# Kernel optimization log

Hardware: AMD Instinct MI355X
Metric: run time of the kernel (lower is better)

The kernel has to match this reference:

```python
import jax, jax.numpy as jnp
import numpy as np

EPS = 1e-12

def _pairwise_dist(a, b):
    # a: [B,N,3], b: [B,M,3] -> Euclidean distances [B,N,M]
    d2 = (jnp.sum(a * a, -1)[:, :, None]
          + jnp.sum(b * b, -1)[:, None, :]
          - 2.0 * jnp.einsum('bnd,bmd->bnm', a, b))
    return jnp.sqrt(jnp.maximum(d2, EPS))


def setup_inputs() -> dict:
    key = jax.random.key(0)
    k1, k2, k3 = jax.random.split(key, 3)
    B, N, M = 16, 4096, 1024
    shape_xyz = jax.random.normal(k1, (B, N, 6), dtype=jnp.float32)
    skel_xyz = jax.random.normal(k2, (B, M, 3), dtype=jnp.float32)
    skel_nori = jax.random.normal(k3, (B, M, 3), dtype=jnp.float32)
    return {"shape_xyz": shape_xyz, "skel_xyz": skel_xyz, "skel_nori": skel_nori}


def reference(shape_xyz, skel_xyz, skel_nori):
    normal = shape_xyz[:, :, 3:6]          # [B,N,3]
    pts = shape_xyz[:, :, :3]              # [B,N,3]
    B = skel_nori.shape[0]

    # Chamfer-style closest distances (sum of min Euclidean distances, both ways)
    d_shape2skel = _pairwise_dist(pts, skel_xyz)   # [B,N,M]
    cd1 = jnp.sum(jnp.min(d_shape2skel, axis=2))
    cd2 = jnp.sum(jnp.min(d_shape2skel, axis=1))   # same matrix transposed
    loss_cd = (cd1 + cd2) * 0.0001

    # KNN (k=2) of each skeletal point among shape points (cKDTree equivalent)
    d_skel2shape = jnp.transpose(d_shape2skel, (0, 2, 1))  # [B,M,N]
    _, idx = jax.lax.top_k(-d_skel2shape, 2)               # [B,M,2]

    # Gather normals of the 2 nearest shape points: [B,M,2,3]
    knn_normals = jnp.take_along_axis(normal[:, None, :, :],
                                      idx[:, :, :, None], axis=2)
    dots = jnp.einsum('bmd,bmkd->bmk', skel_nori, knn_normals)  # [B,M,2]
    # |dot| averaged over k, summed over (b, j), divided by batch size
    loss_normal = jnp.sum(jnp.mean(jnp.abs(dots), axis=-1)) / B

    return loss_cd + 0.001 * loss_normal
```

## Files before the change

### kernel.cpp

```cpp
#include <hip/hip_runtime.h>
#include <cfloat>
#include <stdint.h>

#define B_ 16
#define N_ 4096
#define M_ 1024
#define EPS_ 1e-12f

__device__ __forceinline__ uint32_t umin3(uint32_t a, uint32_t b, uint32_t c) {
    return min(a, min(b, c));
}
__device__ __forceinline__ uint32_t umed3(uint32_t a, uint32_t b, uint32_t c) {
    return max(min(a, b), min(max(a, b), c));
}

__global__ __launch_bounds__(256, 8) void fused_kernel(const float* __restrict__ shape_xyz,
                                                       const float* __restrict__ skel_xyz,
                                                       const float* __restrict__ skel_nori,
                                                       float* __restrict__ out)
{
    __shared__ float4 ls4[1024];
    __shared__ float ws[4];

    const int role = blockIdx.x & 1;
    const int id   = blockIdx.x >> 1;
    const int b    = id >> 6;
    const int sub  = id & 63;

    float v = 0.0f;

    if (role == 0) {
        const float* skb = skel_xyz + (size_t)b * M_ * 3;
        for (int i = threadIdx.x; i < M_; i += 256) {
            const float x = skb[i * 3 + 0];
            const float y = skb[i * 3 + 1];
            const float z = skb[i * 3 + 2];
            ls4[i] = make_float4(x, y, z, fmaf(x, x, fmaf(y, y, z * z)));
        }
        __syncthreads();

        const int s  = threadIdx.x & 15;
        const int g  = threadIdx.x >> 4;
        const int n0 = sub * 64 + g * 4;

        const float* p = shape_xyz + ((size_t)b * N_ + n0) * 6;
        float m2x[4], m2y[4], m2z[4], pp[4], best[4];
#pragma unroll
        for (int k = 0; k < 4; ++k) {
            const float x = p[k * 6 + 0];
            const float y = p[k * 6 + 1];
            const float z = p[k * 6 + 2];
            m2x[k] = -2.0f * x; m2y[k] = -2.0f * y; m2z[k] = -2.0f * z;
            pp[k]  = fmaf(x, x, fmaf(y, y, z * z));
            best[k] = FLT_MAX;
        }

#pragma unroll 4
        for (int t = 0; t < 32; ++t) {
            const float4 sv0 = ls4[t * 32 + s];
            const float4 sv1 = ls4[t * 32 + 16 + s];
#pragma unroll
            for (int k = 0; k < 4; ++k) {
                const float t0 = fmaf(m2x[k], sv0.x, fmaf(m2y[k], sv0.y, fmaf(m2z[k], sv0.z, sv0.w)));
                const float t1 = fmaf(m2x[k], sv1.x, fmaf(m2y[k], sv1.y, fmaf(m2z[k], sv1.z, sv1.w)));
                best[k] = fminf(best[k], fminf(t0, t1));
            }
        }

#pragma unroll
        for (int off = 1; off < 16; off <<= 1) {
#pragma unroll
            for (int k = 0; k < 4; ++k) best[k] = fminf(best[k], __shfl_xor(best[k], off));
        }
        if (s == 0) {
#pragma unroll
            for (int k = 0; k < 4; ++k) v += sqrtf(fmaxf(best[k] + pp[k], EPS_));
            v *= 1e-4f;
        }
    } else {
        const int s  = threadIdx.x & 63;
        const int w  = threadIdx.x >> 6;
        const int m0 = sub * 16 + w * 4;

        float m2x[4], m2y[4], m2z[4], aa[4];
        uint32_t k1[4], k2[4];
        {
            const float* sq = skel_xyz + ((size_t)b * M_ + m0) * 3;
#pragma unroll
            for (int c = 0; c < 4; ++c) {
                const float x = sq[c * 3 + 0];
                const float y = sq[c * 3 + 1];
                const float z = sq[c * 3 + 2];
                m2x[c] = -2.0f * x; m2y[c] = -2.0f * y; m2z[c] = -2.0f * z;
                aa[c]  = fmaf(x, x, fmaf(y, y, z * z));
                k1[c] = 0xFFFFFFFFu; k2[c] = 0xFFFFFFFFu;
            }
        }

        const uint32_t HI = 0xFFFFF000u;
        const float* sb = shape_xyz + (size_t)b * N_ * 6;

        for (int ph = 0; ph < 4; ++ph) {
            __syncthreads();
            for (int i = threadIdx.x; i < 1024; i += 256) {
                const float* pt = sb + (size_t)(ph * 1024 + i) * 6;
                const float x = pt[0], y = pt[1], z = pt[2];
                ls4[i] = make_float4(x, y, z, fmaf(x, x, fmaf(y, y, z * z)));
            }
            __syncthreads();
            const uint32_t nb = (uint32_t)(ph * 1024);

#pragma unroll 2
            for (int j = 0; j < 8; ++j) {
                const int nl = j * 128 + s;
                const float4 qA = ls4[nl];
                const float4 qB = ls4[nl + 64];
                const uint32_t gnA = nb + (uint32_t)nl;
                const uint32_t gnB = gnA + 64u;
#pragma unroll
                for (int c = 0; c < 4; ++c) {
                    const float tA = fmaf(m2x[c], qA.x, fmaf(m2y[c], qA.y, fmaf(m2z[c], qA.z, qA.w + aa[c])));
                    const float tB = fmaf(m2x[c], qB.x, fmaf(m2y[c], qB.y, fmaf(m2z[c], qB.z, qB.w + aa[c])));
                    const uint32_t kA = (__float_as_uint(tA) & HI) | gnA;
                    const uint32_t kB = (__float_as_uint(tB) & HI) | gnB;
                    k2[c] = min(k2[c], umed3(k1[c], kA, kB));
                    k1[c] = umin3(k1[c], kA, kB);
                }
            }
        }

#pragma unroll
        for (int off = 1; off < 64; off <<= 1) {
#pragma unroll
            for (int c = 0; c < 4; ++c) {
                const uint32_t o1 = (uint32_t)__shfl_xor((int)k1[c], off);
                const uint32_t o2 = (uint32_t)__shfl_xor((int)k2[c], off);
                const uint32_t nk2 = min(min(k2[c], o2), max(k1[c], o1));
                k1[c] = min(k1[c], o1);
                k2[c] = nk2;
            }
        }

        if (s == 0) {
            const float* no = skel_nori + ((size_t)b * M_ + m0) * 3;
            const float kN = 0.001f * 0.5f / (float)B_;
#pragma unroll
            for (int c = 0; c < 4; ++c) {
                const int i1 = (int)(k1[c] & 0xFFFu);
                const int i2 = (int)(k2[c] & 0xFFFu);
                const float* p1 = sb + (size_t)i1 * 6;
                const float* p2 = sb + (size_t)i2 * 6;
                const float ax = -0.5f * m2x[c], ay = -0.5f * m2y[c], az = -0.5f * m2z[c];
                const float dx = ax - p1[0], dy = ay - p1[1], dz = az - p1[2];
                const float d2 = fmaf(dx, dx, fmaf(dy, dy, dz * dz));
                const float q0 = no[c * 3 + 0], q1 = no[c * 3 + 1], q2 = no[c * 3 + 2];
                const float dot1 = q0 * p1[3] + q1 * p1[4] + q2 * p1[5];
                const float dot2 = q0 * p2[3] + q1 * p2[4] + q2 * p2[5];
                v += sqrtf(fmaxf(d2, EPS_)) * 1e-4f + (fabsf(dot1) + fabsf(dot2)) * kN;
            }
        }
    }

#pragma unroll
    for (int off = 32; off > 0; off >>= 1) v += __shfl_down(v, off);
    if ((threadIdx.x & 63) == 0) ws[threadIdx.x >> 6] = v;
    __syncthreads();
    if (threadIdx.x == 0) atomicAdd(out, ws[0] + ws[1] + ws[2] + ws[3]);
}

extern "C" void kernel_launch(void* const* d_in, const int* in_sizes, int n_in,
                              void* d_out, int out_size, void* d_ws, size_t ws_size,
                              hipStream_t stream) {
    const float* shape_xyz = (const float*)d_in[0];
    const float* skel_xyz  = (const float*)d_in[1];
    const float* skel_nori = (const float*)d_in[2];
    float* out = (float*)d_out;

    hipMemsetAsync(out, 0, sizeof(float), stream);
    fused_kernel<<<2048, 256, 0, stream>>>(shape_xyz, skel_xyz, skel_nori, out);
}
```

Measured before the change: 93.26 us.

## Merge both distance passes into every block instead of role-split blocks

Instead of alternating blocks between the shape-to-skeleton min pass and the skeleton-to-shape top-2 pass, every block now does a slice of both: 32 shape points against all skeleton points, then 8 skeleton points against all shape points. Each thread now handles 1 shape point and 2 skeleton queries instead of 4, which lowers register pressure and balances work across blocks. The cost is less register-level reuse of each shared-memory load (fewer FMAs per LDS read) and more staging passes overall, since every block now fills shared memory five times.

Result: slower. 98.18 us (+5.3%).

```diff
diff --git a/kernel.cpp b/kernel.cpp
--- a/kernel.cpp
+++ b/kernel.cpp
@@ -22,142 +22,121 @@
     __shared__ float4 ls4[1024];
     __shared__ float ws[4];
 
-    const int role = blockIdx.x & 1;
-    const int id   = blockIdx.x >> 1;
-    const int b    = id >> 6;
-    const int sub  = id & 63;
+    const int b = blockIdx.x >> 7;
+    const int t = blockIdx.x & 127;
 
     float v = 0.0f;
 
-    if (role == 0) {
-        const float* skb = skel_xyz + (size_t)b * M_ * 3;
-        for (int i = threadIdx.x; i < M_; i += 256) {
-            const float x = skb[i * 3 + 0];
-            const float y = skb[i * 3 + 1];
-            const float z = skb[i * 3 + 2];
+    const float* skb = skel_xyz + (size_t)b * M_ * 3;
+    for (int i = threadIdx.x; i < 1024; i += 256) {
+        const float x = skb[i * 3 + 0];
+        const float y = skb[i * 3 + 1];
+        const float z = skb[i * 3 + 2];
+        ls4[i] = make_float4(x, y, z, fmaf(x, x, fmaf(y, y, z * z)));
+    }
+    __syncthreads();
+
+    {
+        const int sA = threadIdx.x & 7;
+        const int gA = threadIdx.x >> 3;
+        const float* p = shape_xyz + ((size_t)b * N_ + t * 32 + gA) * 6;
+        const float px = p[0], py = p[1], pz = p[2];
+        const float m2x = -2.0f * px, m2y = -2.0f * py, m2z = -2.0f * pz;
+        const float pp  = fmaf(px, px, fmaf(py, py, pz * pz));
+
+        float best = FLT_MAX;
+#pragma unroll 4
+        for (int j = 0; j < 64; ++j) {
+            const float4 s0 = ls4[j * 16 + sA];
+            const float4 s1 = ls4[j * 16 + 8 + sA];
+            const float t0 = fmaf(m2x, s0.x, fmaf(m2y, s0.y, fmaf(m2z, s0.z, s0.w)));
+            const float t1 = fmaf(m2x, s1.x, fmaf(m2y, s1.y, fmaf(m2z, s1.z, s1.w)));
+            best = fminf(best, fminf(t0, t1));
+        }
+#pragma unroll
+        for (int off = 1; off < 8; off <<= 1) best = fminf(best, __shfl_xor(best, off));
+        if (sA == 0) v += sqrtf(fmaxf(best + pp, EPS_)) * 1e-4f;
+    }
+
+    const int sB = threadIdx.x & 63;
+    const int w  = threadIdx.x >> 6;
+    const int m0 = t * 8 + w * 2;
+
+    float m2x[2], m2y[2], m2z[2], aa[2];
+    uint32_t k1[2], k2[2];
+    {
+        const float* sq = skel_xyz + ((size_t)b * M_ + m0) * 3;
+#pragma unroll
+        for (int c = 0; c < 2; ++c) {
+            const float x = sq[c * 3 + 0];
+            const float y = sq[c * 3 + 1];
+            const float z = sq[c * 3 + 2];
+            m2x[c] = -2.0f * x; m2y[c] = -2.0f * y; m2z[c] = -2.0f * z;
+            aa[c]  = fmaf(x, x, fmaf(y, y, z * z));
+            k1[c] = 0xFFFFFFFFu; k2[c] = 0xFFFFFFFFu;
+        }
+    }
+
+    const uint32_t HI = 0xFFFFF000u;
+    const float* sb = shape_xyz + (size_t)b * N_ * 6;
+
+    for (int ph = 0; ph < 4; ++ph) {
+        __syncthreads();
+        for (int i = threadIdx.x; i < 1024; i += 256) {
+            const float* pt = sb + (size_t)(ph * 1024 + i) * 6;
+            const float x = pt[0], y = pt[1], z = pt[2];
             ls4[i] = make_float4(x, y, z, fmaf(x, x, fmaf(y, y, z * z)));
         }
         __syncthreads();
+        const uint32_t nb = (uint32_t)(ph * 1024);
 
-        const int s  = threadIdx.x & 15;
-        const int g  = threadIdx.x >> 4;
-        const int n0 = sub * 64 + g * 4;
-
-        const float* p = shape_xyz + ((size_t)b * N_ + n0) * 6;
-        float m2x[4], m2y[4], m2z[4], pp[4], best[4];
+#pragma unroll 2
+        for (int j = 0; j < 8; ++j) {
+            const int nl = j * 128 + sB;
+            const float4 qA = ls4[nl];
+            const float4 qB = ls4[nl + 64];
+            const uint32_t gnA = nb + (uint32_t)nl;
+            const uint32_t gnB = gnA + 64u;
 #pragma unroll
-        for (int k = 0; k < 4; ++k) {
-            const float x = p[k * 6 + 0];
-            const float y = p[k * 6 + 1];
-            const float z = p[k * 6 + 2];
-            m2x[k] = -2.0f * x; m2y[k] = -2.0f * y; m2z[k] = -2.0f * z;
-            pp[k]  = fmaf(x, x, fmaf(y, y, z * z));
-            best[k] = FLT_MAX;
-        }
-
-#pragma unroll 4
-        for (int t = 0; t < 32; ++t) {
-            const float4 sv0 = ls4[t * 32 + s];
-            const float4 sv1 = ls4[t * 32 + 16 + s];
-#pragma unroll
-            for (int k = 0; k < 4; ++k) {
-                const float t0 = fmaf(m2x[k], sv0.x, fmaf(m2y[k], sv0.y, fmaf(m2z[k], sv0.z, sv0.w)));
-                const float t1 = fmaf(m2x[k], sv1.x, fmaf(m2y[k], sv1.y, fmaf(m2z[k], sv1.z, sv1.w)));
-                best[k] = fminf(best[k], fminf(t0, t1));
+            for (int c = 0; c < 2; ++c) {
+                const float tA = fmaf(m2x[c], qA.x, fmaf(m2y[c], qA.y, fmaf(m2z[c], qA.z, qA.w + aa[c])));
+                const float tB = fmaf(m2x[c], qB.x, fmaf(m2y[c], qB.y, fmaf(m2z[c], qB.z, qB.w + aa[c])));
+                const uint32_t kA = (__float_as_uint(tA) & HI) | gnA;
+                const uint32_t kB = (__float_as_uint(tB) & HI) | gnB;
+                k2[c] = min(k2[c], umed3(k1[c], kA, kB));
+                k1[c] = umin3(k1[c], kA, kB);
             }
         }
+    }
 
 #pragma unroll
-        for (int off = 1; off < 16; off <<= 1) {
+    for (int off = 1; off < 64; off <<= 1) {
 #pragma unroll
-            for (int k = 0; k < 4; ++k) best[k] = fminf(best[k], __shfl_xor(best[k], off));
+        for (int c = 0; c < 2; ++c) {
+            const uint32_t o1 = (uint32_t)__shfl_xor((int)k1[c], off);
+            const uint32_t o2 = (uint32_t)__shfl_xor((int)k2[c], off);
+            const uint32_t nk2 = min(min(k2[c], o2), max(k1[c], o1));
+            k1[c] = min(k1[c], o1);
+            k2[c] = nk2;
         }
-        if (s == 0) {
+    }
+
+    if (sB == 0) {
+        const float* no = skel_nori + ((size_t)b * M_ + m0) * 3;
+        const float kN = 0.001f * 0.5f / (float)B_;
 #pragma unroll
-            for (int k = 0; k < 4; ++k) v += sqrtf(fmaxf(best[k] + pp[k], EPS_));
-            v *= 1e-4f;
-        }
-    } else {
-        const int s  = threadIdx.x & 63;
-        const int w  = threadIdx.x >> 6;
-        const int m0 = sub * 16 + w * 4;
-
-        float m2x[4], m2y[4], m2z[4], aa[4];
-        uint32_t k1[4], k2[4];
-        {
-            const float* sq = skel_xyz + ((size_t)b * M_ + m0) * 3;
-#pragma unroll
-            for (int c = 0; c < 4; ++c) {
-                const float x = sq[c * 3 + 0];
-                const float y = sq[c * 3 + 1];
-                const float z = sq[c * 3 + 2];
-                m2x[c] = -2.0f * x; m2y[c] = -2.0f * y; m2z[c] = -2.0f * z;
-                aa[c]  = fmaf(x, x, fmaf(y, y, z * z));
-                k1[c] = 0xFFFFFFFFu; k2[c] = 0xFFFFFFFFu;
-            }
-        }
-
-        const uint32_t HI = 0xFFFFF000u;
-        const float* sb = shape_xyz + (size_t)b * N_ * 6;
-
-        for (int ph = 0; ph < 4; ++ph) {
-            __syncthreads();
-            for (int i = threadIdx.x; i < 1024; i += 256) {
-                const float* pt = sb + (size_t)(ph * 1024 + i) * 6;
-                const float x = pt[0], y = pt[1], z = pt[2];
-                ls4[i] = make_float4(x, y, z, fmaf(x, x, fmaf(y, y, z * z)));
-            }
-            __syncthreads();
-            const uint32_t nb = (uint32_t)(ph * 1024);
-
-#pragma unroll 2
-            for (int j = 0; j < 8; ++j) {
-                const int nl = j * 128 + s;
-                const float4 qA = ls4[nl];
-                const float4 qB = ls4[nl + 64];
-                const uint32_t gnA = nb + (uint32_t)nl;
-                const uint32_t gnB = gnA + 64u;
-#pragma unroll
-                for (int c = 0; c < 4; ++c) {
-                    const float tA = fmaf(m2x[c], qA.x, fmaf(m2y[c], qA.y, fmaf(m2z[c], qA.z, qA.w + aa[c])));
-                    const float tB = fmaf(m2x[c], qB.x, fmaf(m2y[c], qB.y, fmaf(m2z[c], qB.z, qB.w + aa[c])));
-                    const uint32_t kA = (__float_as_uint(tA) & HI) | gnA;
-                    const uint32_t kB = (__float_as_uint(tB) & HI) | gnB;
-                    k2[c] = min(k2[c], umed3(k1[c], kA, kB));
-                    k1[c] = umin3(k1[c], kA, kB);
-                }
-            }
-        }
-
-#pragma unroll
-        for (int off = 1; off < 64; off <<= 1) {
-#pragma unroll
-            for (int c = 0; c < 4; ++c) {
-                const uint32_t o1 = (uint32_t)__shfl_xor((int)k1[c], off);
-                const uint32_t o2 = (uint32_t)__shfl_xor((int)k2[c], off);
-                const uint32_t nk2 = min(min(k2[c], o2), max(k1[c], o1));
-                k1[c] = min(k1[c], o1);
-                k2[c] = nk2;
-            }
-        }
-
-        if (s == 0) {
-            const float* no = skel_nori + ((size_t)b * M_ + m0) * 3;
-            const float kN = 0.001f * 0.5f / (float)B_;
-#pragma unroll
-            for (int c = 0; c < 4; ++c) {
-                const int i1 = (int)(k1[c] & 0xFFFu);
-                const int i2 = (int)(k2[c] & 0xFFFu);
-                const float* p1 = sb + (size_t)i1 * 6;
-                const float* p2 = sb + (size_t)i2 * 6;
-                const float ax = -0.5f * m2x[c], ay = -0.5f * m2y[c], az = -0.5f * m2z[c];
-                const float dx = ax - p1[0], dy = ay - p1[1], dz = az - p1[2];
-                const float d2 = fmaf(dx, dx, fmaf(dy, dy, dz * dz));
-                const float q0 = no[c * 3 + 0], q1 = no[c * 3 + 1], q2 = no[c * 3 + 2];
-                const float dot1 = q0 * p1[3] + q1 * p1[4] + q2 * p1[5];
-                const float dot2 = q0 * p2[3] + q1 * p2[4] + q2 * p2[5];
-                v += sqrtf(fmaxf(d2, EPS_)) * 1e-4f + (fabsf(dot1) + fabsf(dot2)) * kN;
-            }
+        for (int c = 0; c < 2; ++c) {
+            const int i1 = (int)(k1[c] & 0xFFFu);
+            const int i2 = (int)(k2[c] & 0xFFFu);
+            const float* p1 = sb + (size_t)i1 * 6;
+            const float* p2 = sb + (size_t)i2 * 6;
+            const float ax = -0.5f * m2x[c], ay = -0.5f * m2y[c], az = -0.5f * m2z[c];
+            const float dx = ax - p1[0], dy = ay - p1[1], dz = az - p1[2];
+            const float d2 = fmaf(dx, dx, fmaf(dy, dy, dz * dz));
+            const float q0 = no[c * 3 + 0], q1 = no[c * 3 + 1], q2 = no[c * 3 + 2];
+            const float dot1 = q0 * p1[3] + q1 * p1[4] + q2 * p1[5];
+            const float dot2 = q0 * p2[3] + q1 * p2[4] + q2 * p2[5];
+            v += sqrtf(fmaxf(d2, EPS_)) * 1e-4f + (fabsf(dot1) + fabsf(dot2)) * kN;
         }
     }
 
```

## Rebalance chamfer/KNN block split, vectorize staging loads, prefetch next KNN phase

Applied to the files above, without the earlier changes.

The grid drops from 2048 to 1536 blocks. There are now 512 chamfer blocks, each handling 8 shape points per thread, and 1024 KNN blocks using 32-lane groups with 2 skeleton points each. Global staging of skeleton and shape coordinates now uses float4 loads that are unpacked into the LDS tile. The KNN path prefetches the next phase's shape tile into registers while it computes the current one. Launch bounds are lowered to 6 waves to allow more registers. The cost is fewer KNN queries per LDS read, so LDS traffic per FMA rises on that path, and occupancy may drop.

Result: faster. 87.46 us (-6.2%).

```diff
diff --git a/kernel.cpp b/kernel.cpp
--- a/kernel.cpp
+++ b/kernel.cpp
@@ -14,7 +14,7 @@
     return max(min(a, b), min(max(a, b), c));
 }
 
-__global__ __launch_bounds__(256, 8) void fused_kernel(const float* __restrict__ shape_xyz,
+__global__ __launch_bounds__(256, 6) void fused_kernel(const float* __restrict__ shape_xyz,
                                                        const float* __restrict__ skel_xyz,
                                                        const float* __restrict__ skel_nori,
                                                        float* __restrict__ out)
@@ -22,31 +22,26 @@
     __shared__ float4 ls4[1024];
     __shared__ float ws[4];
 
-    const int role = blockIdx.x & 1;
-    const int id   = blockIdx.x >> 1;
-    const int b    = id >> 6;
-    const int sub  = id & 63;
-
+    const int tid = threadIdx.x;
     float v = 0.0f;
 
-    if (role == 0) {
-        const float* skb = skel_xyz + (size_t)b * M_ * 3;
-        for (int i = threadIdx.x; i < M_; i += 256) {
-            const float x = skb[i * 3 + 0];
-            const float y = skb[i * 3 + 1];
-            const float z = skb[i * 3 + 2];
-            ls4[i] = make_float4(x, y, z, fmaf(x, x, fmaf(y, y, z * z)));
-        }
-        __syncthreads();
-
-        const int s  = threadIdx.x & 15;
-        const int g  = threadIdx.x >> 4;
-        const int n0 = sub * 64 + g * 4;
-
+    if (blockIdx.x < 512) {
+        const int id  = blockIdx.x;
+        const int b   = id >> 5;
+        const int sub = id & 31;
+
+        const float4* g4 = (const float4*)(skel_xyz + (size_t)b * M_ * 3);
+        const float4 r0 = g4[3 * tid + 0];
+        const float4 r1 = g4[3 * tid + 1];
+        const float4 r2 = g4[3 * tid + 2];
+
+        const int sA = tid & 15;
+        const int gA = tid >> 4;
+        const int n0 = sub * 128 + gA * 8;
         const float* p = shape_xyz + ((size_t)b * N_ + n0) * 6;
-        float m2x[4], m2y[4], m2z[4], pp[4], best[4];
-#pragma unroll
-        for (int k = 0; k < 4; ++k) {
+        float m2x[8], m2y[8], m2z[8], pp[8], best[8];
+#pragma unroll
+        for (int k = 0; k < 8; ++k) {
             const float x = p[k * 6 + 0];
             const float y = p[k * 6 + 1];
             const float z = p[k * 6 + 2];
@@ -55,14 +50,27 @@
             best[k] = FLT_MAX;
         }
 
+        {
+            float x, y, z;
+            x = r0.x; y = r0.y; z = r0.z;
+            ls4[4 * tid + 0] = make_float4(x, y, z, fmaf(x, x, fmaf(y, y, z * z)));
+            x = r0.w; y = r1.x; z = r1.y;
+            ls4[4 * tid + 1] = make_float4(x, y, z, fmaf(x, x, fmaf(y, y, z * z)));
+            x = r1.z; y = r1.w; z = r2.x;
+            ls4[4 * tid + 2] = make_float4(x, y, z, fmaf(x, x, fmaf(y, y, z * z)));
+            x = r2.y; y = r2.z; z = r2.w;
+            ls4[4 * tid + 3] = make_float4(x, y, z, fmaf(x, x, fmaf(y, y, z * z)));
+        }
+        __syncthreads();
+
 #pragma unroll 4
-        for (int t = 0; t < 32; ++t) {
-            const float4 sv0 = ls4[t * 32 + s];
-            const float4 sv1 = ls4[t * 32 + 16 + s];
-#pragma unroll
-            for (int k = 0; k < 4; ++k) {
-                const float t0 = fmaf(m2x[k], sv0.x, fmaf(m2y[k], sv0.y, fmaf(m2z[k], sv0.z, sv0.w)));
-                const float t1 = fmaf(m2x[k], sv1.x, fmaf(m2y[k], sv1.y, fmaf(m2z[k], sv1.z, sv1.w)));
+        for (int j = 0; j < 32; ++j) {
+            const float4 s0 = ls4[j * 32 + sA];
+            const float4 s1 = ls4[j * 32 + 16 + sA];
+#pragma unroll
+            for (int k = 0; k < 8; ++k) {
+                const float t0 = fmaf(m2x[k], s0.x, fmaf(m2y[k], s0.y, fmaf(m2z[k], s0.z, s0.w)));
+                const float t1 = fmaf(m2x[k], s1.x, fmaf(m2y[k], s1.y, fmaf(m2z[k], s1.z, s1.w)));
                 best[k] = fminf(best[k], fminf(t0, t1));
             }
         }
@@ -70,24 +78,27 @@
 #pragma unroll
         for (int off = 1; off < 16; off <<= 1) {
 #pragma unroll
-            for (int k = 0; k < 4; ++k) best[k] = fminf(best[k], __shfl_xor(best[k], off));
-        }
-        if (s == 0) {
-#pragma unroll
-            for (int k = 0; k < 4; ++k) v += sqrtf(fmaxf(best[k] + pp[k], EPS_));
+            for (int k = 0; k < 8; ++k) best[k] = fminf(best[k], __shfl_xor(best[k], off));
+        }
+        if (sA == 0) {
+#pragma unroll
+            for (int k = 0; k < 8; ++k) v += sqrtf(fmaxf(best[k] + pp[k], EPS_));
             v *= 1e-4f;
         }
     } else {
-        const int s  = threadIdx.x & 63;
-        const int w  = threadIdx.x >> 6;
-        const int m0 = sub * 16 + w * 4;
-
-        float m2x[4], m2y[4], m2z[4], aa[4];
-        uint32_t k1[4], k2[4];
+        const int id  = blockIdx.x - 512;
+        const int b   = id >> 6;
+        const int sub = id & 63;
+        const int s   = tid & 31;
+        const int g   = tid >> 5;
+        const int m0  = sub * 16 + g * 2;
+
+        float m2x[2], m2y[2], m2z[2], aa[2];
+        uint32_t k1[2], k2[2];
         {
             const float* sq = skel_xyz + ((size_t)b * M_ + m0) * 3;
 #pragma unroll
-            for (int c = 0; c < 4; ++c) {
+            for (int c = 0; c < 2; ++c) {
                 const float x = sq[c * 3 + 0];
                 const float y = sq[c * 3 + 1];
                 const float z = sq[c * 3 + 2];
@@ -99,40 +110,54 @@
 
         const uint32_t HI = 0xFFFFF000u;
         const float* sb = shape_xyz + (size_t)b * N_ * 6;
+        const float4* g4 = (const float4*)sb;
+
+        float4 r[6];
+#pragma unroll
+        for (int k = 0; k < 6; ++k) r[k] = g4[6 * tid + k];
 
         for (int ph = 0; ph < 4; ++ph) {
             __syncthreads();
-            for (int i = threadIdx.x; i < 1024; i += 256) {
-                const float* pt = sb + (size_t)(ph * 1024 + i) * 6;
-                const float x = pt[0], y = pt[1], z = pt[2];
-                ls4[i] = make_float4(x, y, z, fmaf(x, x, fmaf(y, y, z * z)));
+            {
+                float x, y, z;
+                x = r[0].x; y = r[0].y; z = r[0].z;
+                ls4[4 * tid + 0] = make_float4(x, y, z, fmaf(x, x, fmaf(y, y, z * z)));
+                x = r[1].z; y = r[1].w; z = r[2].x;
+                ls4[4 * tid + 1] = make_float4(x, y, z, fmaf(x, x, fmaf(y, y, z * z)));
+                x = r[3].x; y = r[3].y; z = r[3].z;
+                ls4[4 * tid + 2] = make_float4(x, y, z, fmaf(x, x, fmaf(y, y, z * z)));
+                x = r[4].z; y = r[4].w; z = r[5].x;
+                ls4[4 * tid + 3] = make_float4(x, y, z, fmaf(x, x, fmaf(y, y, z * z)));
             }
             __syncthreads();
+            if (ph < 3) {
+#pragma unroll
+                for (int k = 0; k < 6; ++k) r[k] = g4[(ph + 1) * 1536 + 6 * tid + k];
+            }
             const uint32_t nb = (uint32_t)(ph * 1024);
 
-#pragma unroll 2
-            for (int j = 0; j < 8; ++j) {
-                const int nl = j * 128 + s;
-                const float4 qA = ls4[nl];
-                const float4 qB = ls4[nl + 64];
-                const uint32_t gnA = nb + (uint32_t)nl;
-                const uint32_t gnB = gnA + 64u;
-#pragma unroll
-                for (int c = 0; c < 4; ++c) {
-                    const float tA = fmaf(m2x[c], qA.x, fmaf(m2y[c], qA.y, fmaf(m2z[c], qA.z, qA.w + aa[c])));
-                    const float tB = fmaf(m2x[c], qB.x, fmaf(m2y[c], qB.y, fmaf(m2z[c], qB.z, qB.w + aa[c])));
-                    const uint32_t kA = (__float_as_uint(tA) & HI) | gnA;
-                    const uint32_t kB = (__float_as_uint(tB) & HI) | gnB;
-                    k2[c] = min(k2[c], umed3(k1[c], kA, kB));
-                    k1[c] = umin3(k1[c], kA, kB);
+#pragma unroll 4
+            for (int j = 0; j < 16; ++j) {
+                const float4 q0 = ls4[j * 64 + s];
+                const float4 q1 = ls4[j * 64 + 32 + s];
+                const uint32_t gn0 = nb + (uint32_t)(j * 64 + s);
+                const uint32_t gn1 = gn0 + 32u;
+#pragma unroll
+                for (int c = 0; c < 2; ++c) {
+                    const float t0 = fmaf(m2x[c], q0.x, fmaf(m2y[c], q0.y, fmaf(m2z[c], q0.z, q0.w + aa[c])));
+                    const float t1 = fmaf(m2x[c], q1.x, fmaf(m2y[c], q1.y, fmaf(m2z[c], q1.z, q1.w + aa[c])));
+                    const uint32_t kk0 = (__float_as_uint(t0) & HI) | gn0;
+                    const uint32_t kk1 = (__float_as_uint(t1) & HI) | gn1;
+                    k2[c] = min(k2[c], umed3(k1[c], kk0, kk1));
+                    k1[c] = umin3(k1[c], kk0, kk1);
                 }
             }
         }
 
 #pragma unroll
-        for (int off = 1; off < 64; off <<= 1) {
-#pragma unroll
-            for (int c = 0; c < 4; ++c) {
+        for (int off = 1; off < 32; off <<= 1) {
+#pragma unroll
+            for (int c = 0; c < 2; ++c) {
                 const uint32_t o1 = (uint32_t)__shfl_xor((int)k1[c], off);
                 const uint32_t o2 = (uint32_t)__shfl_xor((int)k2[c], off);
                 const uint32_t nk2 = min(min(k2[c], o2), max(k1[c], o1));
@@ -145,7 +170,7 @@
             const float* no = skel_nori + ((size_t)b * M_ + m0) * 3;
             const float kN = 0.001f * 0.5f / (float)B_;
 #pragma unroll
-            for (int c = 0; c < 4; ++c) {
+            for (int c = 0; c < 2; ++c) {
                 const int i1 = (int)(k1[c] & 0xFFFu);
                 const int i2 = (int)(k2[c] & 0xFFFu);
                 const float* p1 = sb + (size_t)i1 * 6;
@@ -163,9 +188,9 @@
 
 #pragma unroll
     for (int off = 32; off > 0; off >>= 1) v += __shfl_down(v, off);
-    if ((threadIdx.x & 63) == 0) ws[threadIdx.x >> 6] = v;
+    if ((tid & 63) == 0) ws[tid >> 6] = v;
     __syncthreads();
-    if (threadIdx.x == 0) atomicAdd(out, ws[0] + ws[1] + ws[2] + ws[3]);
+    if (tid == 0) atomicAdd(out, ws[0] + ws[1] + ws[2] + ws[3]);
 }
 
 extern "C" void kernel_launch(void* const* d_in, const int* in_sizes, int n_in,
@@ -177,5 +202,5 @@
     float* out = (float*)d_out;
 
     hipMemsetAsync(out, 0, sizeof(float), stream);
-    fused_kernel<<<2048, 256, 0, stream>>>(shape_xyz, skel_xyz, skel_nori, out);
-}
+    fused_kernel<<<1536, 256, 0, stream>>>(shape_xyz, skel_xyz, skel_nori, out);
+}
```
